# Optimization experiments

Hardware: AMD Instinct MI355X
Metric: run time of the kernel (lower is better)

## Reference

```python
import jax, jax.numpy as jnp
import numpy as np

WINDOW = 128
CAUSAL = True
LOOK_BACKWARD = 1
LOOK_FORWARD = 0  # causal forces look_forward = 0


def _look_around(x, backward, forward, pad_value, dim):
    # pad along window axis (axis=1), then concat shifted slices along `dim`
    nw = x.shape[1]
    pad_cfg = [(0, 0)] * x.ndim
    pad_cfg[1] = (backward, forward)
    padded = jnp.pad(x, pad_cfg, constant_values=pad_value)
    slices = [padded[:, i:i + nw] for i in range(forward + backward + 1)]
    return jnp.concatenate(slices, axis=dim)


def setup_inputs() -> dict:
    key = jax.random.key(0)
    kq, kk, kv = jax.random.split(key, 3)
    shape = (2, 16, 4096, 64)
    return {
        "q": jax.random.normal(kq, shape, dtype=jnp.float32),
        "k": jax.random.normal(kk, shape, dtype=jnp.float32),
        "v": jax.random.normal(kv, shape, dtype=jnp.float32),
    }


def reference(q, k, v):
    b, h, t, e = q.shape
    scale = e ** (-0.5)
    windows = t // WINDOW  # t assumed divisible by WINDOW (pad_to_multiple is no-op)

    # merge batch and heads, bucket into windows
    bq = q.reshape(b * h, windows, WINDOW, e)
    bk = k.reshape(b * h, windows, WINDOW, e)
    bv = v.reshape(b * h, windows, WINDOW, e)

    # look-around gather of key/value windows: j-dim = WINDOW*(1+back+fwd)
    bk = _look_around(bk, LOOK_BACKWARD, LOOK_FORWARD, 0.0, dim=2)
    bv = _look_around(bv, LOOK_BACKWARD, LOOK_FORWARD, 0.0, dim=2)

    # positional indices for masking
    bq_t = jnp.arange(t).reshape(1, windows, WINDOW)
    bq_k = _look_around(bq_t, LOOK_BACKWARD, LOOK_FORWARD, -1, dim=2)

    mask = (bq_k == -1)[:, :, None, :]  # (1, w, 1, j) padded positions
    if CAUSAL:
        mask = mask | (bq_t[:, :, :, None] < bq_k[:, :, None, :])

    dots = jnp.einsum('bwie,bwje->bwij', bq * scale, bk)
    mask_value = -jnp.finfo(dots.dtype).max
    dots = jnp.where(mask, mask_value, dots)
    attn = jax.nn.softmax(dots.astype(jnp.float32), axis=-1).astype(dots.dtype)
    out = jnp.einsum('bwij,bwje->bwie', attn, bv)
    return out.reshape(b, h, t, e)
```

## Files before the change

kernel.cpp:

```cpp
#include <hip/hip_runtime.h>

#define T_DIM 4096
#define E_DIM 64
#define WIN   128
#define NWIN  (T_DIM / WIN)
#define KS_LD 72
#define VT_LD 136

typedef __bf16  bf16x8 __attribute__((ext_vector_type(8)));
typedef __bf16  bf16x4 __attribute__((ext_vector_type(4)));
typedef float   f32x16 __attribute__((ext_vector_type(16)));

#if defined(__has_builtin) && __has_builtin(__builtin_amdgcn_permlane32_swap)
typedef int v2i_t __attribute__((ext_vector_type(2)));
__device__ __forceinline__ void lane32_swap(unsigned &a, unsigned &b) {
  v2i_t r = __builtin_amdgcn_permlane32_swap((int)a, (int)b, false, false);
  a = (unsigned)r.x; b = (unsigned)r.y;
}
#else
__device__ __forceinline__ void lane32_swap(unsigned &a, unsigned &b) {
  const bool lo = ((threadIdx.x & 63) < 32);
  const unsigned pa = __shfl_xor(a, 32), pb = __shfl_xor(b, 32);
  const unsigned na = lo ? a : pb;
  const unsigned nb = lo ? pa : b;
  a = na; b = nb;
}
#endif

__global__ __launch_bounds__(256, 4)
void la_fwd(const float* __restrict__ Q, const float* __restrict__ K,
            const float* __restrict__ V, float* __restrict__ O)
{
  __shared__ __bf16 Ks[WIN * KS_LD];
  __shared__ __bf16 Vt[E_DIM * VT_LD];

  const int tid  = threadIdx.x;
  const int lane = tid & 63;
  const int wid  = tid >> 6;
  const int col  = lane & 31;
  const int half = lane >> 5;

  const int w  = blockIdx.x;
  const int bh = blockIdx.y;

  const float* Qb = Q + (size_t)bh * T_DIM * E_DIM;
  const float* Kb = K + (size_t)bh * T_DIM * E_DIM;
  const float* Vb = V + (size_t)bh * T_DIM * E_DIM;
  float*       Ob = O + (size_t)bh * T_DIM * E_DIM;

  const int q0 = w * WIN;

  const float QS = 0.125f * 1.44269504088896340736f;
  bf16x8 aq[4];
  {
    const float* qrow = Qb + (size_t)(q0 + wid * 32 + col) * E_DIM;
#pragma unroll
    for (int c = 0; c < 4; ++c) {
      const float* p = qrow + c * 16 + half * 8;
      const float4 x = *(const float4*)(p);
      const float4 y = *(const float4*)(p + 4);
      bf16x8 a;
      a[0]=(__bf16)(x.x*QS); a[1]=(__bf16)(x.y*QS); a[2]=(__bf16)(x.z*QS); a[3]=(__bf16)(x.w*QS);
      a[4]=(__bf16)(y.x*QS); a[5]=(__bf16)(y.y*QS); a[6]=(__bf16)(y.z*QS); a[7]=(__bf16)(y.w*QS);
      aq[c] = a;
    }
  }

  float lr = 0.0f;
  f32x16 oacc[2];
#pragma unroll
  for (int et = 0; et < 2; ++et)
#pragma unroll
    for (int r = 0; r < 16; ++r) oacc[et][r] = 0.0f;

  auto stage = [&](int kr0) {
    const float* kp = Kb + (size_t)kr0 * E_DIM;
#pragma unroll 4
    for (int i = 0; i < 8; ++i) {
      const int fi = (i << 10) + (tid << 2);
      const float4 kv = *(const float4*)(kp + fi);
      const int row = fi >> 6, cole = fi & 63;
      bf16x4 k4; k4[0]=(__bf16)kv.x; k4[1]=(__bf16)kv.y; k4[2]=(__bf16)kv.z; k4[3]=(__bf16)kv.w;
      *(bf16x4*)(&Ks[row * KS_LD + cole]) = k4;
    }
    const int j  = tid & 127;
    const int ch = (tid >> 7) * 32;
    const float* vrow = Vb + (size_t)(kr0 + j) * E_DIM + ch;
#pragma unroll 4
    for (int c4 = 0; c4 < 8; ++c4) {
      const float4 vv = *(const float4*)(vrow + c4 * 4);
      const int e = ch + c4 * 4;
      Vt[(e + 0) * VT_LD + j] = (__bf16)vv.x;
      Vt[(e + 1) * VT_LD + j] = (__bf16)vv.y;
      Vt[(e + 2) * VT_LD + j] = (__bf16)vv.z;
      Vt[(e + 3) * VT_LD + j] = (__bf16)vv.w;
    }
  };

  auto kb_step = [&](int kb, bool diag) {
    f32x16 s;
#pragma unroll
    for (int r = 0; r < 16; ++r) s[r] = 0.0f;
#pragma unroll
    for (int c = 0; c < 4; ++c) {
      const bf16x8 ak = *(const bf16x8*)(&Ks[(kb * 32 + col) * KS_LD + c * 16 + half * 8]);
      s = __builtin_amdgcn_mfma_f32_32x32x16_bf16(ak, aq[c], s, 0, 0, 0);
    }
#pragma unroll
    for (int r = 0; r < 16; ++r) {
      const int kk = (r & 3) + 8 * (r >> 2) + 4 * half;
      float sv = s[r];
      if (diag && kk > col) sv = -3.0e38f;
      const float p = __builtin_amdgcn_exp2f(sv);
      lr += p;
      s[r] = p;
    }
    unsigned pk8[8];
#pragma unroll
    for (int g = 0; g < 8; ++g) {
      union { __bf16 h[2]; unsigned u; } pu;
      pu.h[0] = (__bf16)s[2 * g];
      pu.h[1] = (__bf16)s[2 * g + 1];
      pk8[g] = pu.u;
    }
#pragma unroll
    for (int c2 = 0; c2 < 2; ++c2) {
      unsigned b0 = pk8[4 * c2 + 0], b1 = pk8[4 * c2 + 1];
      unsigned b2 = pk8[4 * c2 + 2], b3 = pk8[4 * c2 + 3];
      lane32_swap(b0, b2);
      lane32_swap(b1, b3);
      union { unsigned u[4]; bf16x8 v; } bf;
      bf.u[0] = b0; bf.u[1] = b1; bf.u[2] = b2; bf.u[3] = b3;
      const int j0 = kb * 32 + c2 * 16 + half * 8;
#pragma unroll
      for (int et = 0; et < 2; ++et) {
        const bf16x8 av = *(const bf16x8*)(&Vt[(et * 32 + col) * VT_LD + j0]);
        oacc[et] = __builtin_amdgcn_mfma_f32_32x32x16_bf16(av, bf.v, oacc[et], 0, 0, 0);
      }
    }
  };

  if (w > 0) {
    stage(q0 - WIN);
    __syncthreads();
#pragma unroll
    for (int kb = 0; kb < 4; ++kb) kb_step(kb, false);
    __syncthreads();
  }

  stage(q0);
  __syncthreads();
  for (int kb = 0; kb <= wid; ++kb) kb_step(kb, kb == wid);

  const float ltot = lr + __shfl_xor(lr, 32);
  const float rinv = __builtin_amdgcn_rcpf(ltot);
  float* op = Ob + (size_t)(q0 + wid * 32 + col) * E_DIM;
#pragma unroll
  for (int et = 0; et < 2; ++et)
#pragma unroll
    for (int g = 0; g < 4; ++g) {
      float4 o4;
      o4.x = oacc[et][4 * g + 0] * rinv;
      o4.y = oacc[et][4 * g + 1] * rinv;
      o4.z = oacc[et][4 * g + 2] * rinv;
      o4.w = oacc[et][4 * g + 3] * rinv;
      *(float4*)(op + et * 32 + 8 * g + 4 * half) = o4;
    }
}

extern "C" void kernel_launch(void* const* d_in, const int* in_sizes, int n_in,
                              void* d_out, int out_size, void* d_ws, size_t ws_size,
                              hipStream_t stream) {
  const float* Q = (const float*)d_in[0];
  const float* K = (const float*)d_in[1];
  const float* V = (const float*)d_in[2];
  float*       O = (float*)d_out;
  const int bh = in_sizes[0] / (T_DIM * E_DIM);
  dim3 grid(NWIN, bh);
  la_fwd<<<grid, 256, 0, stream>>>(Q, K, V, O);
}
```

Before: 147.6 us.

## Coalesce V loads via row-major staging then in-LDS transpose; swap grid axes

```diff
diff --git a/kernel.cpp b/kernel.cpp
--- a/kernel.cpp
+++ b/kernel.cpp
@@ -31,8 +31,8 @@
 void la_fwd(const float* __restrict__ Q, const float* __restrict__ K,
             const float* __restrict__ V, float* __restrict__ O)
 {
-  __shared__ __bf16 Ks[WIN * KS_LD];
-  __shared__ __bf16 Vt[E_DIM * VT_LD];
+  __shared__ __attribute__((aligned(16))) __bf16 Ks[WIN * KS_LD];
+  __shared__ __attribute__((aligned(16))) __bf16 VB[WIN * KS_LD];
 
   const int tid  = threadIdx.x;
   const int lane = tid & 63;
@@ -40,8 +40,8 @@
   const int col  = lane & 31;
   const int half = lane >> 5;
 
-  const int w  = blockIdx.x;
-  const int bh = blockIdx.y;
+  const int bh = blockIdx.x;
+  const int w  = blockIdx.y;
 
   const float* Qb = Q + (size_t)bh * T_DIM * E_DIM;
   const float* Kb = K + (size_t)bh * T_DIM * E_DIM;
@@ -73,28 +73,36 @@
 #pragma unroll
     for (int r = 0; r < 16; ++r) oacc[et][r] = 0.0f;
 
-  auto stage = [&](int kr0) {
+  auto stageKV = [&](int kr0) {
     const float* kp = Kb + (size_t)kr0 * E_DIM;
+    const float* vp = Vb + (size_t)kr0 * E_DIM;
 #pragma unroll 4
     for (int i = 0; i < 8; ++i) {
       const int fi = (i << 10) + (tid << 2);
       const float4 kv = *(const float4*)(kp + fi);
+      const float4 vv = *(const float4*)(vp + fi);
       const int row = fi >> 6, cole = fi & 63;
       bf16x4 k4; k4[0]=(__bf16)kv.x; k4[1]=(__bf16)kv.y; k4[2]=(__bf16)kv.z; k4[3]=(__bf16)kv.w;
+      bf16x4 v4; v4[0]=(__bf16)vv.x; v4[1]=(__bf16)vv.y; v4[2]=(__bf16)vv.z; v4[3]=(__bf16)vv.w;
       *(bf16x4*)(&Ks[row * KS_LD + cole]) = k4;
+      *(bf16x4*)(&VB[row * KS_LD + cole]) = v4;
     }
+  };
+
+  auto transposeV = [&]() {
     const int j  = tid & 127;
-    const int ch = (tid >> 7) * 32;
-    const float* vrow = Vb + (size_t)(kr0 + j) * E_DIM + ch;
-#pragma unroll 4
-    for (int c4 = 0; c4 < 8; ++c4) {
-      const float4 vv = *(const float4*)(vrow + c4 * 4);
-      const int e = ch + c4 * 4;
-      Vt[(e + 0) * VT_LD + j] = (__bf16)vv.x;
-      Vt[(e + 1) * VT_LD + j] = (__bf16)vv.y;
-      Vt[(e + 2) * VT_LD + j] = (__bf16)vv.z;
-      Vt[(e + 3) * VT_LD + j] = (__bf16)vv.w;
-    }
+    const int e0 = (tid >> 7) * 32;
+    bf16x8 tv[4];
+#pragma unroll
+    for (int g = 0; g < 4; ++g)
+      tv[g] = *(const bf16x8*)(&VB[j * KS_LD + e0 + 8 * g]);
+    __syncthreads();
+#pragma unroll
+    for (int g = 0; g < 4; ++g)
+#pragma unroll
+      for (int m = 0; m < 8; ++m)
+        VB[(e0 + 8 * g + m) * VT_LD + j] = tv[g][m];
+    __syncthreads();
   };
 
   auto kb_step = [&](int kb, bool diag) {
@@ -134,22 +142,24 @@
       const int j0 = kb * 32 + c2 * 16 + half * 8;
 #pragma unroll
       for (int et = 0; et < 2; ++et) {
-        const bf16x8 av = *(const bf16x8*)(&Vt[(et * 32 + col) * VT_LD + j0]);
+        const bf16x8 av = *(const bf16x8*)(&VB[(et * 32 + col) * VT_LD + j0]);
         oacc[et] = __builtin_amdgcn_mfma_f32_32x32x16_bf16(av, bf.v, oacc[et], 0, 0, 0);
       }
     }
   };
 
   if (w > 0) {
-    stage(q0 - WIN);
+    stageKV(q0 - WIN);
     __syncthreads();
+    transposeV();
 #pragma unroll
     for (int kb = 0; kb < 4; ++kb) kb_step(kb, false);
     __syncthreads();
   }
 
-  stage(q0);
+  stageKV(q0);
   __syncthreads();
+  transposeV();
   for (int kb = 0; kb <= wid; ++kb) kb_step(kb, kb == wid);
 
   const float ltot = lr + __shfl_xor(lr, 32);
@@ -176,6 +186,6 @@
   const float* V = (const float*)d_in[2];
   float*       O = (float*)d_out;
   const int bh = in_sizes[0] / (T_DIM * E_DIM);
-  dim3 grid(NWIN, bh);
+  dim3 grid(bh, NWIN);
   la_fwd<<<grid, 256, 0, stream>>>(Q, K, V, O);
 }
```

Result: no change. 148.6 us (+0.7%).
